# Optimization experiments

Hardware: AMD Instinct MI355X
Metric: run time of the kernel (lower is better)

## Reference

```python
import jax, jax.numpy as jnp
import numpy as np

B, A, N_IN, N_HID, N_OUT, MAX_Z = 2048, 96, 128, 64, 1, 100
SHIFT = float(np.log(2.0))

def ssp(x):
    # shifted softplus: softplus(x) - log(2)
    return jax.nn.softplus(x) - SHIFT

def setup_inputs() -> dict:
    key = jax.random.key(0)
    ks = jax.random.split(key, 8)
    rep = jax.random.normal(ks[0], (B, A, N_IN), dtype=jnp.float32)
    atomic_numbers = jax.random.randint(ks[1], (B, A), 0, MAX_Z)
    atom_mask = jnp.ones((B, A), dtype=jnp.float32)
    s1 = 1.0 / np.sqrt(N_IN)
    s2 = 1.0 / np.sqrt(N_HID)
    W1 = jax.random.uniform(ks[2], (N_IN, N_HID), jnp.float32, -s1, s1)
    b1 = jax.random.uniform(ks[3], (N_HID,), jnp.float32, -s1, s1)
    W2 = jax.random.uniform(ks[4], (N_HID, N_OUT), jnp.float32, -s2, s2)
    b2 = jax.random.uniform(ks[5], (N_OUT,), jnp.float32, -s2, s2)
    atomref_table = jax.random.normal(ks[6], (MAX_Z, N_OUT), dtype=jnp.float32) * 0.1
    atomref_table = atomref_table.at[0].set(0.0)  # mask-atom reference is zero
    mean = jnp.array([0.0], dtype=jnp.float32)
    stddev = jnp.array([1.0], dtype=jnp.float32)
    return {"representation": rep, "atomic_numbers": atomic_numbers,
            "atom_mask": atom_mask, "W1": W1, "b1": b1, "W2": W2, "b2": b2,
            "atomref_table": atomref_table, "mean": mean, "stddev": stddev}

def reference(representation, atomic_numbers, atom_mask, W1, b1, W2, b2,
              atomref_table, mean, stddev):
    # per-atom MLP: [B,A,n_in] -> [B,A,n_out]
    h = ssp(jnp.einsum('bai,ih->bah', representation, W1) + b1)
    yi = jnp.einsum('bah,ho->bao', h, W2) + b2
    # standardize (ScaleShift): y * stddev + mean
    yi = yi * stddev + mean
    # atomref embedding lookup and add
    yi = yi + atomref_table[atomic_numbers]  # [B,A,n_out]
    # masked sum aggregation over atoms (Aggregate axis=1, mean=False)
    y = jnp.sum(yi * atom_mask[..., None], axis=1)  # [B,n_out]
    return y
```

## Files before the change

### kernel.cpp

```cpp
#include <hip/hip_runtime.h>
#include <hip/hip_bf16.h>

#define BB 2048
#define AA 96
#define NIN 128
#define NHID 64

typedef __attribute__((ext_vector_type(8))) short bf16x8;
typedef __attribute__((ext_vector_type(4))) float f32x4;

static __device__ __forceinline__ unsigned short f2bf(float x) {
    unsigned u = __builtin_bit_cast(unsigned, x);
    return (unsigned short)((u + 0x7FFFu + ((u >> 16) & 1u)) >> 16);
}
static __device__ __forceinline__ unsigned cvt_pk_hw(float a, float b) {
    __hip_bfloat162 h = __float22bfloat162_rn(make_float2(a, b));
    unsigned u; __builtin_memcpy(&u, &h, 4);
    return u;
}

__global__ void prep_kernel(const float* __restrict__ w1,
                            const float* __restrict__ b1,
                            const float* __restrict__ w2,
                            unsigned char* __restrict__ ws,
                            float* __restrict__ out, int out_n) {
    const int gid = blockIdx.x * 256 + threadIdx.x;
    if (gid < 1024) {
        const int lane = gid & 63, st = gid >> 6;
        const int s = st >> 2, t = st & 3;
        const int k0 = s * 32 + (lane >> 4) * 8;
        const int n  = t * 16 + (lane & 15);
        unsigned short o[8];
        #pragma unroll
        for (int j = 0; j < 8; ++j) o[j] = f2bf(w1[(k0 + j) * NHID + n]);
        uint4 v; __builtin_memcpy(&v, o, 16);
        ((uint4*)ws)[gid] = v;
    } else if (gid < 1088) {
        ((float*)(ws + 16384))[gid - 1024] = b1[gid - 1024];
    } else if (gid < 1152) {
        ((float*)(ws + 16640))[gid - 1088] = w2[gid - 1088];
    } else if (gid - 1152 < out_n) {
        out[gid - 1152] = 0.0f;
    }
}

__global__ __launch_bounds__(256, 4) void atomwise_kernel(
    const float* __restrict__ rep,
    const int*   __restrict__ zs,
    const float* __restrict__ mask,
    const unsigned char* __restrict__ ws,
    const float* __restrict__ b2,
    const float* __restrict__ aref,
    const float* __restrict__ mean,
    const float* __restrict__ stddev,
    float* __restrict__ out)
{
    const int tid  = threadIdx.x;
    const int lane = tid & 63;
    const int wv   = tid >> 6;
    const int nl   = lane & 15;
    const int quad = lane >> 4;
    const int atom0 = (blockIdx.x * 4 + wv) * 16;

    const float* rowp = rep + (size_t)(atom0 + nl) * NIN + quad * 8;
    float4 q[8];
    #pragma unroll
    for (int s = 0; s < 4; ++s) {
        q[2 * s]     = *(const float4*)(rowp + s * 32);
        q[2 * s + 1] = *(const float4*)(rowp + s * 32 + 4);
    }

    const int   ag    = atom0 + quad * 4 + (nl & 3);
    const float mq    = mask[ag];
    const float arefv = aref[zs[ag]];

    const bf16x8* w1f = (const bf16x8*)ws;
    const float*  b1s = (const float*)(ws + 16384);
    const float*  w2s = (const float*)(ws + 16640);

    float b1v[4], w2v[4];
    #pragma unroll
    for (int t = 0; t < 4; ++t) {
        b1v[t] = b1s[t * 16 + nl];
        w2v[t] = w2s[t * 16 + nl];
    }

    const float sdv  = stddev[0];
    const float cadd = fmaf(b2[0], sdv, mean[0]);
    const float LOG2E = 1.4426950408889634f;
    const float LN2   = 0.6931471805599453f;

    f32x4 acc[4];
    #pragma unroll
    for (int t = 0; t < 4; ++t) acc[t] = (f32x4){0.f, 0.f, 0.f, 0.f};

    #pragma unroll
    for (int s = 0; s < 4; ++s) {
        union { bf16x8 v; unsigned u[4]; } fa;
        fa.u[0] = cvt_pk_hw(q[2 * s].x,     q[2 * s].y);
        fa.u[1] = cvt_pk_hw(q[2 * s].z,     q[2 * s].w);
        fa.u[2] = cvt_pk_hw(q[2 * s + 1].x, q[2 * s + 1].y);
        fa.u[3] = cvt_pk_hw(q[2 * s + 1].z, q[2 * s + 1].w);
        const bf16x8* fr = &w1f[s * 256 + lane];
        #pragma unroll
        for (int t = 0; t < 4; ++t)
            acc[t] = __builtin_amdgcn_mfma_f32_16x16x32_bf16(fa.v, fr[t * 64], acc[t], 0, 0, 0);
    }

    float v[4];
    #pragma unroll
    for (int r = 0; r < 4; ++r) {
        float p = 0.f;
        #pragma unroll
        for (int t = 0; t < 4; ++t) {
            float x  = acc[t][r] + b1v[t];
            float ax = fabsf(x);
            float em = exp2f(-ax * LOG2E);
            float sp = fmaxf(x, 0.f) + log2f(1.f + em) * LN2;
            p = fmaf(sp - LN2, w2v[t], p);
        }
        p += __shfl_xor(p, 1); p += __shfl_xor(p, 2);
        p += __shfl_xor(p, 4); p += __shfl_xor(p, 8);
        v[r] = p;
    }

    const int rsel = nl & 3;
    float vr = v[0];
    vr = rsel == 1 ? v[1] : vr;
    vr = rsel == 2 ? v[2] : vr;
    vr = rsel == 3 ? v[3] : vr;
    float contrib = (nl < 4) ? mq * (fmaf(vr, sdv, cadd) + arefv) : 0.f;
    #pragma unroll
    for (int off = 32; off; off >>= 1) contrib += __shfl_xor(contrib, off);
    if (lane == 0) atomicAdd(out + atom0 / AA, contrib);
}

extern "C" void kernel_launch(void* const* d_in, const int* in_sizes, int n_in,
                              void* d_out, int out_size, void* d_ws, size_t ws_size,
                              hipStream_t stream) {
    const float* rep    = (const float*)d_in[0];
    const int*   zs     = (const int*)  d_in[1];
    const float* mask   = (const float*)d_in[2];
    const float* w1     = (const float*)d_in[3];
    const float* b1     = (const float*)d_in[4];
    const float* w2     = (const float*)d_in[5];
    const float* b2     = (const float*)d_in[6];
    const float* aref   = (const float*)d_in[7];
    const float* mean   = (const float*)d_in[8];
    const float* stddev = (const float*)d_in[9];
    float* out = (float*)d_out;
    unsigned char* ws = (unsigned char*)d_ws;

    const int prep_threads = 1152 + out_size;
    const int prep_blocks  = (prep_threads + 255) / 256;
    prep_kernel<<<dim3(prep_blocks), dim3(256), 0, stream>>>(w1, b1, w2, ws, out, out_size);

    const int blocks = (BB * AA) / (4 * 16);
    atomwise_kernel<<<dim3(blocks), dim3(256), 0, stream>>>(
        rep, zs, mask, ws, b2, aref, mean, stddev, out);
}
```

Before: 166.2 us.

## Process two atom tiles per wave with LDS-staged weights and nontemporal loads

```diff
diff --git a/kernel.cpp b/kernel.cpp
--- a/kernel.cpp
+++ b/kernel.cpp
@@ -44,69 +44,12 @@
     }
 }
 
-__global__ __launch_bounds__(256, 4) void atomwise_kernel(
-    const float* __restrict__ rep,
-    const int*   __restrict__ zs,
-    const float* __restrict__ mask,
-    const unsigned char* __restrict__ ws,
-    const float* __restrict__ b2,
-    const float* __restrict__ aref,
-    const float* __restrict__ mean,
-    const float* __restrict__ stddev,
-    float* __restrict__ out)
-{
-    const int tid  = threadIdx.x;
-    const int lane = tid & 63;
-    const int wv   = tid >> 6;
-    const int nl   = lane & 15;
-    const int quad = lane >> 4;
-    const int atom0 = (blockIdx.x * 4 + wv) * 16;
-
-    const float* rowp = rep + (size_t)(atom0 + nl) * NIN + quad * 8;
-    float4 q[8];
-    #pragma unroll
-    for (int s = 0; s < 4; ++s) {
-        q[2 * s]     = *(const float4*)(rowp + s * 32);
-        q[2 * s + 1] = *(const float4*)(rowp + s * 32 + 4);
-    }
-
-    const int   ag    = atom0 + quad * 4 + (nl & 3);
-    const float mq    = mask[ag];
-    const float arefv = aref[zs[ag]];
-
-    const bf16x8* w1f = (const bf16x8*)ws;
-    const float*  b1s = (const float*)(ws + 16384);
-    const float*  w2s = (const float*)(ws + 16640);
-
-    float b1v[4], w2v[4];
-    #pragma unroll
-    for (int t = 0; t < 4; ++t) {
-        b1v[t] = b1s[t * 16 + nl];
-        w2v[t] = w2s[t * 16 + nl];
-    }
-
-    const float sdv  = stddev[0];
-    const float cadd = fmaf(b2[0], sdv, mean[0]);
+static __device__ __forceinline__ float tile_reduce(const f32x4* acc,
+                                                    const float* b1v,
+                                                    const float* w2v,
+                                                    int nl) {
     const float LOG2E = 1.4426950408889634f;
     const float LN2   = 0.6931471805599453f;
-
-    f32x4 acc[4];
-    #pragma unroll
-    for (int t = 0; t < 4; ++t) acc[t] = (f32x4){0.f, 0.f, 0.f, 0.f};
-
-    #pragma unroll
-    for (int s = 0; s < 4; ++s) {
-        union { bf16x8 v; unsigned u[4]; } fa;
-        fa.u[0] = cvt_pk_hw(q[2 * s].x,     q[2 * s].y);
-        fa.u[1] = cvt_pk_hw(q[2 * s].z,     q[2 * s].w);
-        fa.u[2] = cvt_pk_hw(q[2 * s + 1].x, q[2 * s + 1].y);
-        fa.u[3] = cvt_pk_hw(q[2 * s + 1].z, q[2 * s + 1].w);
-        const bf16x8* fr = &w1f[s * 256 + lane];
-        #pragma unroll
-        for (int t = 0; t < 4; ++t)
-            acc[t] = __builtin_amdgcn_mfma_f32_16x16x32_bf16(fa.v, fr[t * 64], acc[t], 0, 0, 0);
-    }
-
     float v[4];
     #pragma unroll
     for (int r = 0; r < 4; ++r) {
@@ -123,13 +66,108 @@
         p += __shfl_xor(p, 4); p += __shfl_xor(p, 8);
         v[r] = p;
     }
-
     const int rsel = nl & 3;
     float vr = v[0];
     vr = rsel == 1 ? v[1] : vr;
     vr = rsel == 2 ? v[2] : vr;
     vr = rsel == 3 ? v[3] : vr;
-    float contrib = (nl < 4) ? mq * (fmaf(vr, sdv, cadd) + arefv) : 0.f;
+    return vr;
+}
+
+__global__ __launch_bounds__(256, 3) void atomwise_kernel(
+    const float* __restrict__ rep,
+    const int*   __restrict__ zs,
+    const float* __restrict__ mask,
+    const unsigned char* __restrict__ ws,
+    const float* __restrict__ b2,
+    const float* __restrict__ aref,
+    const float* __restrict__ mean,
+    const float* __restrict__ stddev,
+    float* __restrict__ out)
+{
+    __shared__ unsigned char smem[16896];
+
+    const int tid  = threadIdx.x;
+    const int lane = tid & 63;
+    const int wv   = tid >> 6;
+    const int nl   = lane & 15;
+    const int quad = lane >> 4;
+    const int atom0 = (blockIdx.x * 4 + wv) * 32;
+
+    {
+        const uint4* src = (const uint4*)ws;
+        uint4*       dst = (uint4*)smem;
+        #pragma unroll
+        for (int i = 0; i < 4; ++i) dst[tid + i * 256] = src[tid + i * 256];
+        if (tid < 32) dst[1024 + tid] = src[1024 + tid];
+    }
+    __syncthreads();
+
+    const int   ag0   = atom0 + quad * 4 + (nl & 3);
+    const int   ag1   = ag0 + 16;
+    const float mq0   = mask[ag0];
+    const float mq1   = mask[ag1];
+    const float aref0 = aref[zs[ag0]];
+    const float aref1 = aref[zs[ag1]];
+
+    const float* rowp0 = rep + (size_t)(atom0 + nl) * NIN + quad * 8;
+    const float* rowp1 = rowp0 + 16 * NIN;
+    f32x4 q0[8], q1[8];
+    #pragma unroll
+    for (int s = 0; s < 4; ++s) {
+        q0[2 * s]     = __builtin_nontemporal_load((const f32x4*)(rowp0 + s * 32));
+        q0[2 * s + 1] = __builtin_nontemporal_load((const f32x4*)(rowp0 + s * 32 + 4));
+        q1[2 * s]     = __builtin_nontemporal_load((const f32x4*)(rowp1 + s * 32));
+        q1[2 * s + 1] = __builtin_nontemporal_load((const f32x4*)(rowp1 + s * 32 + 4));
+    }
+
+    const bf16x8* w1f = (const bf16x8*)smem;
+    const float*  b1s = (const float*)(smem + 16384);
+    const float*  w2s = (const float*)(smem + 16640);
+
+    float b1v[4], w2v[4];
+    #pragma unroll
+    for (int t = 0; t < 4; ++t) {
+        b1v[t] = b1s[t * 16 + nl];
+        w2v[t] = w2s[t * 16 + nl];
+    }
+
+    const float sdv  = stddev[0];
+    const float cadd = fmaf(b2[0], sdv, mean[0]);
+
+    f32x4 acc0[4], acc1[4];
+    #pragma unroll
+    for (int t = 0; t < 4; ++t) {
+        acc0[t] = (f32x4){0.f, 0.f, 0.f, 0.f};
+        acc1[t] = (f32x4){0.f, 0.f, 0.f, 0.f};
+    }
+
+    #pragma unroll
+    for (int s = 0; s < 4; ++s) {
+        union { bf16x8 v; unsigned u[4]; } fa0, fa1;
+        fa0.u[0] = cvt_pk_hw(q0[2 * s].x,     q0[2 * s].y);
+        fa0.u[1] = cvt_pk_hw(q0[2 * s].z,     q0[2 * s].w);
+        fa0.u[2] = cvt_pk_hw(q0[2 * s + 1].x, q0[2 * s + 1].y);
+        fa0.u[3] = cvt_pk_hw(q0[2 * s + 1].z, q0[2 * s + 1].w);
+        fa1.u[0] = cvt_pk_hw(q1[2 * s].x,     q1[2 * s].y);
+        fa1.u[1] = cvt_pk_hw(q1[2 * s].z,     q1[2 * s].w);
+        fa1.u[2] = cvt_pk_hw(q1[2 * s + 1].x, q1[2 * s + 1].y);
+        fa1.u[3] = cvt_pk_hw(q1[2 * s + 1].z, q1[2 * s + 1].w);
+        const bf16x8* fr = &w1f[s * 256 + lane];
+        #pragma unroll
+        for (int t = 0; t < 4; ++t) {
+            bf16x8 w = fr[t * 64];
+            acc0[t] = __builtin_amdgcn_mfma_f32_16x16x32_bf16(fa0.v, w, acc0[t], 0, 0, 0);
+            acc1[t] = __builtin_amdgcn_mfma_f32_16x16x32_bf16(fa1.v, w, acc1[t], 0, 0, 0);
+        }
+    }
+
+    const float vr0 = tile_reduce(acc0, b1v, w2v, nl);
+    const float vr1 = tile_reduce(acc1, b1v, w2v, nl);
+
+    float c0 = (nl < 4) ? mq0 * (fmaf(vr0, sdv, cadd) + aref0) : 0.f;
+    float c1 = (nl < 4) ? mq1 * (fmaf(vr1, sdv, cadd) + aref1) : 0.f;
+    float contrib = c0 + c1;
     #pragma unroll
     for (int off = 32; off; off >>= 1) contrib += __shfl_xor(contrib, off);
     if (lane == 0) atomicAdd(out + atom0 / AA, contrib);
@@ -155,7 +193,7 @@
     const int prep_blocks  = (prep_threads + 255) / 256;
     prep_kernel<<<dim3(prep_blocks), dim3(256), 0, stream>>>(w1, b1, w2, ws, out, out_size);
 
-    const int blocks = (BB * AA) / (4 * 16);
+    const int blocks = (BB * AA) / (4 * 32);
     atomwise_kernel<<<dim3(blocks), dim3(256), 0, stream>>>(
         rep, zs, mask, ws, b2, aref, mean, stddev, out);
 }
```

Result: no change. 163.9 us (-1.4%).

## Fuse weight prep into main kernel with one block per molecule

Applied to the files above, without the earlier changes.

```diff
diff --git a/kernel.cpp b/kernel.cpp
--- a/kernel.cpp
+++ b/kernel.cpp
@@ -9,86 +9,115 @@
 typedef __attribute__((ext_vector_type(8))) short bf16x8;
 typedef __attribute__((ext_vector_type(4))) float f32x4;
 
-static __device__ __forceinline__ unsigned short f2bf(float x) {
-    unsigned u = __builtin_bit_cast(unsigned, x);
-    return (unsigned short)((u + 0x7FFFu + ((u >> 16) & 1u)) >> 16);
-}
 static __device__ __forceinline__ unsigned cvt_pk_hw(float a, float b) {
     __hip_bfloat162 h = __float22bfloat162_rn(make_float2(a, b));
     unsigned u; __builtin_memcpy(&u, &h, 4);
     return u;
 }
 
-__global__ void prep_kernel(const float* __restrict__ w1,
-                            const float* __restrict__ b1,
-                            const float* __restrict__ w2,
-                            unsigned char* __restrict__ ws,
-                            float* __restrict__ out, int out_n) {
-    const int gid = blockIdx.x * 256 + threadIdx.x;
-    if (gid < 1024) {
-        const int lane = gid & 63, st = gid >> 6;
-        const int s = st >> 2, t = st & 3;
-        const int k0 = s * 32 + (lane >> 4) * 8;
-        const int n  = t * 16 + (lane & 15);
-        unsigned short o[8];
+static __device__ __forceinline__ float tile_reduce(const f32x4* acc,
+                                                    const float* b1v,
+                                                    const float* w2v,
+                                                    int nl) {
+    const float LOG2E = 1.4426950408889634f;
+    const float LN2   = 0.6931471805599453f;
+    float v[4];
+    #pragma unroll
+    for (int r = 0; r < 4; ++r) {
+        float p = 0.f;
         #pragma unroll
-        for (int j = 0; j < 8; ++j) o[j] = f2bf(w1[(k0 + j) * NHID + n]);
-        uint4 v; __builtin_memcpy(&v, o, 16);
-        ((uint4*)ws)[gid] = v;
-    } else if (gid < 1088) {
-        ((float*)(ws + 16384))[gid - 1024] = b1[gid - 1024];
-    } else if (gid < 1152) {
-        ((float*)(ws + 16640))[gid - 1088] = w2[gid - 1088];
-    } else if (gid - 1152 < out_n) {
-        out[gid - 1152] = 0.0f;
+        for (int t = 0; t < 4; ++t) {
+            float x  = acc[t][r] + b1v[t];
+            float ax = fabsf(x);
+            float em = exp2f(-ax * LOG2E);
+            float sp = fmaxf(x, 0.f) + log2f(1.f + em) * LN2;
+            p = fmaf(sp - LN2, w2v[t], p);
+        }
+        p += __shfl_xor(p, 1); p += __shfl_xor(p, 2);
+        p += __shfl_xor(p, 4); p += __shfl_xor(p, 8);
+        v[r] = p;
     }
+    const int rsel = nl & 3;
+    float vr = v[0];
+    vr = rsel == 1 ? v[1] : vr;
+    vr = rsel == 2 ? v[2] : vr;
+    vr = rsel == 3 ? v[3] : vr;
+    return vr;
 }
 
-__global__ __launch_bounds__(256, 4) void atomwise_kernel(
+__global__ __launch_bounds__(384, 4) void atomwise_kernel(
     const float* __restrict__ rep,
     const int*   __restrict__ zs,
     const float* __restrict__ mask,
-    const unsigned char* __restrict__ ws,
+    const float* __restrict__ w1,
+    const float* __restrict__ b1,
+    const float* __restrict__ w2,
     const float* __restrict__ b2,
     const float* __restrict__ aref,
     const float* __restrict__ mean,
     const float* __restrict__ stddev,
     float* __restrict__ out)
 {
+    __shared__ unsigned char smem[16928];
+
     const int tid  = threadIdx.x;
     const int lane = tid & 63;
     const int wv   = tid >> 6;
     const int nl   = lane & 15;
     const int quad = lane >> 4;
-    const int atom0 = (blockIdx.x * 4 + wv) * 16;
+    const int mol  = blockIdx.x;
+    const int atomb = mol * AA + wv * 16;
 
-    const float* rowp = rep + (size_t)(atom0 + nl) * NIN + quad * 8;
-    float4 q[8];
+    {
+        uint4* dst = (uint4*)smem;
+        #pragma unroll
+        for (int it = 0; it < 3; ++it) {
+            const int fid = tid + it * 384;
+            if (fid < 1024) {
+                const int fl = fid & 63, st = fid >> 6;
+                const int s = st >> 2, t = st & 3;
+                const int k0 = s * 32 + (fl >> 4) * 8;
+                const int n  = t * 16 + (fl & 15);
+                const float* wp = w1 + k0 * NHID + n;
+                float e[8];
+                #pragma unroll
+                for (int j = 0; j < 8; ++j) e[j] = wp[j * NHID];
+                uint4 v;
+                v.x = cvt_pk_hw(e[0], e[1]);
+                v.y = cvt_pk_hw(e[2], e[3]);
+                v.z = cvt_pk_hw(e[4], e[5]);
+                v.w = cvt_pk_hw(e[6], e[7]);
+                dst[fid] = v;
+            }
+        }
+        if (tid < 64)       ((float*)(smem + 16384))[tid]      = b1[tid];
+        else if (tid < 128) ((float*)(smem + 16640))[tid - 64] = w2[tid - 64];
+    }
+    __syncthreads();
+
+    const float* rowp = rep + (size_t)(atomb + nl) * NIN + quad * 8;
+    f32x4 q[8];
     #pragma unroll
     for (int s = 0; s < 4; ++s) {
-        q[2 * s]     = *(const float4*)(rowp + s * 32);
-        q[2 * s + 1] = *(const float4*)(rowp + s * 32 + 4);
+        q[2 * s]     = __builtin_nontemporal_load((const f32x4*)(rowp + s * 32));
+        q[2 * s + 1] = __builtin_nontemporal_load((const f32x4*)(rowp + s * 32 + 4));
     }
 
-    const int   ag    = atom0 + quad * 4 + (nl & 3);
+    const int   ag    = atomb + quad * 4 + (nl & 3);
     const float mq    = mask[ag];
     const float arefv = aref[zs[ag]];
+    const float sdv   = stddev[0];
+    const float cadd  = fmaf(b2[0], sdv, mean[0]);
 
-    const bf16x8* w1f = (const bf16x8*)ws;
-    const float*  b1s = (const float*)(ws + 16384);
-    const float*  w2s = (const float*)(ws + 16640);
-
+    const bf16x8* w1f = (const bf16x8*)smem;
+    const float*  b1s = (const float*)(smem + 16384);
+    const float*  w2s = (const float*)(smem + 16640);
     float b1v[4], w2v[4];
     #pragma unroll
     for (int t = 0; t < 4; ++t) {
         b1v[t] = b1s[t * 16 + nl];
         w2v[t] = w2s[t * 16 + nl];
     }
-
-    const float sdv  = stddev[0];
-    const float cadd = fmaf(b2[0], sdv, mean[0]);
-    const float LOG2E = 1.4426950408889634f;
-    const float LN2   = 0.6931471805599453f;
 
     f32x4 acc[4];
     #pragma unroll
@@ -107,32 +136,20 @@
             acc[t] = __builtin_amdgcn_mfma_f32_16x16x32_bf16(fa.v, fr[t * 64], acc[t], 0, 0, 0);
     }
 
-    float v[4];
-    #pragma unroll
-    for (int r = 0; r < 4; ++r) {
-        float p = 0.f;
-        #pragma unroll
-        for (int t = 0; t < 4; ++t) {
-            float x  = acc[t][r] + b1v[t];
-            float ax = fabsf(x);
-            float em = exp2f(-ax * LOG2E);
-            float sp = fmaxf(x, 0.f) + log2f(1.f + em) * LN2;
-            p = fmaf(sp - LN2, w2v[t], p);
-        }
-        p += __shfl_xor(p, 1); p += __shfl_xor(p, 2);
-        p += __shfl_xor(p, 4); p += __shfl_xor(p, 8);
-        v[r] = p;
-    }
+    const float vr = tile_reduce(acc, b1v, w2v, nl);
 
-    const int rsel = nl & 3;
-    float vr = v[0];
-    vr = rsel == 1 ? v[1] : vr;
-    vr = rsel == 2 ? v[2] : vr;
-    vr = rsel == 3 ? v[3] : vr;
     float contrib = (nl < 4) ? mq * (fmaf(vr, sdv, cadd) + arefv) : 0.f;
     #pragma unroll
     for (int off = 32; off; off >>= 1) contrib += __shfl_xor(contrib, off);
-    if (lane == 0) atomicAdd(out + atom0 / AA, contrib);
+    float* scratch = (float*)(smem + 16896);
+    if (lane == 0) scratch[wv] = contrib;
+    __syncthreads();
+
+    if (tid == 0) {
+        float tot = scratch[0] + scratch[1] + scratch[2]
+                  + scratch[3] + scratch[4] + scratch[5];
+        out[mol] = tot;
+    }
 }
 
 extern "C" void kernel_launch(void* const* d_in, const int* in_sizes, int n_in,
@@ -149,13 +166,7 @@
     const float* mean   = (const float*)d_in[8];
     const float* stddev = (const float*)d_in[9];
     float* out = (float*)d_out;
-    unsigned char* ws = (unsigned char*)d_ws;
 
-    const int prep_threads = 1152 + out_size;
-    const int prep_blocks  = (prep_threads + 255) / 256;
-    prep_kernel<<<dim3(prep_blocks), dim3(256), 0, stream>>>(w1, b1, w2, ws, out, out_size);
-
-    const int blocks = (BB * AA) / (4 * 16);
-    atomwise_kernel<<<dim3(blocks), dim3(256), 0, stream>>>(
-        rep, zs, mask, ws, b2, aref, mean, stddev, out);
+    atomwise_kernel<<<dim3(BB), dim3(384), 0, stream>>>(
+        rep, zs, mask, w1, b1, w2, b2, aref, mean, stddev, out);
 }
```

Measured after the change: 165.1 us. No clear change (-0.7%).
